# Kernel tuning notes

Measured on AMD Instinct MI355X. Metric: run time of the kernel, lower is better.

The kernel has to match this reference:

```python
import jax, jax.numpy as jnp
import numpy as np

DIM = 256
WS = 12          # window_size
NH = 8           # num_heads
HD = DIM // NH   # head_dim
NW = WS * WS     # tokens per window = 144


def _relative_position_index(ws: int) -> np.ndarray:
    coords = np.stack(np.meshgrid(np.arange(ws), np.arange(ws), indexing='ij'))  # [2, ws, ws]
    cf = coords.reshape(2, -1)                                  # [2, Nw]
    rel = cf[:, :, None] - cf[:, None, :]                       # [2, Nw, Nw]
    rel = rel.transpose(1, 2, 0).copy()                         # [Nw, Nw, 2]
    rel[:, :, 0] += ws - 1
    rel[:, :, 1] += ws - 1
    rel[:, :, 0] *= 2 * ws - 1
    return rel.sum(-1).astype(np.int32)                         # [Nw, Nw]


def setup_inputs() -> dict:
    key = jax.random.key(0)
    ks = jax.random.split(key, 6)
    BnW = 2048
    x = jax.random.normal(ks[0], (BnW, NW, DIM), dtype=jnp.float32)
    # weights stored as [in, out] (torch Linear applies x @ W.T + b)
    qkv_w = jax.random.normal(ks[1], (DIM, 3 * DIM), dtype=jnp.float32) * 0.02
    qkv_b = jnp.zeros((3 * DIM,), dtype=jnp.float32)
    proj_w = jax.random.normal(ks[2], (DIM, DIM), dtype=jnp.float32) * 0.02
    proj_b = jnp.zeros((DIM,), dtype=jnp.float32)
    rpb_table = jax.random.normal(ks[3], ((2 * WS - 1) ** 2, NH), dtype=jnp.float32) * 0.02
    rel_index = jnp.asarray(_relative_position_index(WS))       # [Nw, Nw] int32
    return {"x": x, "qkv_w": qkv_w, "qkv_b": qkv_b, "proj_w": proj_w,
            "proj_b": proj_b, "rpb_table": rpb_table, "rel_index": rel_index}


def reference(x, qkv_w, qkv_b, proj_w, proj_b, rpb_table, rel_index):
    BnW, Nw, C = x.shape
    scale = HD ** -0.5
    qkv = x @ qkv_w + qkv_b                                     # [BnW, Nw, 3C]
    qkv = qkv.reshape(BnW, Nw, 3, NH, HD)
    q, k, v = qkv[:, :, 0], qkv[:, :, 1], qkv[:, :, 2]          # [BnW, Nw, H, D]
    attn = jnp.einsum('bnhd,bmhd->bhnm', q * scale, k)          # [BnW, H, Nw, Nw]
    bias = rpb_table[rel_index]                                 # [Nw, Nw, H]
    attn = attn + jnp.transpose(bias, (2, 0, 1))[None]          # broadcast over BnW
    attn = jax.nn.softmax(attn, axis=-1)
    out = jnp.einsum('bhnm,bmhd->bnhd', attn, v).reshape(BnW, Nw, C)
    return out @ proj_w + proj_b
```

## Files before the change

kernel.cpp:

```cpp
#include <hip/hip_runtime.h>
#include <cstdint>
#include <cstddef>

#define NWIN 2048
#define NW   144
#define DIM  256
#define NHD  8
#define HD   32
#define MTOT (NWIN * NW)
#define SCALE 0.17677669529663687f

typedef __bf16 bf16x8 __attribute__((ext_vector_type(8)));
typedef float  f32x4  __attribute__((ext_vector_type(4)));
typedef unsigned short u16;
typedef unsigned short u16x4 __attribute__((ext_vector_type(4)));

__device__ __forceinline__ u16 f2bf(float f) {
  unsigned u = __float_as_uint(f);
  u += 0x7fffu + ((u >> 16) & 1u);
  return (u16)(u >> 16);
}

__device__ __forceinline__ bf16x8 pack8(f32x4 lo, f32x4 hi) {
  union { bf16x8 v; u16 u[8]; } o;
  o.u[0] = f2bf(lo.x); o.u[1] = f2bf(lo.y); o.u[2] = f2bf(lo.z); o.u[3] = f2bf(lo.w);
  o.u[4] = f2bf(hi.x); o.u[5] = f2bf(hi.y); o.u[6] = f2bf(hi.z); o.u[7] = f2bf(hi.w);
  return o.v;
}

__device__ __forceinline__ f32x4 mfma16(bf16x8 a, bf16x8 b, f32x4 c) {
  return __builtin_amdgcn_mfma_f32_16x16x32_bf16(a, b, c, 0, 0, 0);
}

__global__ void k_prep(const float* __restrict__ qkv_w, const float* __restrict__ proj_w,
                       const float* __restrict__ rpb, const int* __restrict__ rel,
                       u16* __restrict__ wqkvt, u16* __restrict__ wprojt,
                       float* __restrict__ biasar) {
  int tid = blockIdx.x * blockDim.x + threadIdx.x;
  int stride = gridDim.x * blockDim.x;
  for (int i = tid; i < 768 * 256; i += stride) {
    int n = i >> 8, k = i & 255;
    wqkvt[i] = f2bf(qkv_w[(size_t)k * 768 + n]);
  }
  for (int i = tid; i < 256 * 256; i += stride) {
    int n = i >> 8, k = i & 255;
    wprojt[i] = f2bf(proj_w[(size_t)k * 256 + n]);
  }
  for (int i = tid; i < NW * NW; i += stride) {
    int idv = rel[i];
#pragma unroll
    for (int hh = 0; hh < 8; ++hh) biasar[hh * (NW * NW) + i] = rpb[idv * 8 + hh];
  }
}

template <int NT, bool AF32, bool OUTF32>
__global__ __launch_bounds__(256) void k_gemm_bt(const void* __restrict__ Av,
                                                 const u16* __restrict__ Bt,
                                                 const float* __restrict__ bias,
                                                 void* __restrict__ outv) {
  constexpr int N = NT * 128;
  __shared__ __align__(16) u16 As[128 * 64];
  __shared__ __align__(16) u16 Bs[128 * 64];
  int tid = threadIdx.x;
  int wave = tid >> 6, lane = tid & 63;
  int ln = lane & 15, quad = lane >> 4;
  int wm = wave >> 1, wn = wave & 1;

  int bid = blockIdx.x;
  int xcd = bid & 7, slot = bid >> 3;
  int mt = xcd * 288 + slot / NT;
  int nt = slot % NT;
  int m0 = mt * 128, n0 = nt * 128;

  f32x4 zero4 = {0.f, 0.f, 0.f, 0.f};
  f32x4 acc[4][4];
#pragma unroll
  for (int i = 0; i < 4; ++i)
#pragma unroll
    for (int j = 0; j < 4; ++j) acc[i][j] = zero4;

  for (int kt = 0; kt < 4; ++kt) {
    int k0 = kt * 64;
    bf16x8 avs[4], bvs[4];
#pragma unroll
    for (int i = 0; i < 4; ++i) {
      int s = i * 256 + tid;
      int r = s >> 3, c = s & 7;
      if constexpr (AF32) {
        const float* Af = (const float*)Av;
        const float* p = &Af[(size_t)(m0 + r) * 256 + k0 + c * 8];
        f32x4 lo = *(const f32x4*)p;
        f32x4 hi = *(const f32x4*)(p + 4);
        avs[i] = pack8(lo, hi);
      } else {
        const u16* Ab = (const u16*)Av;
        avs[i] = *(const bf16x8*)&Ab[(size_t)(m0 + r) * 256 + k0 + c * 8];
      }
      bvs[i] = *(const bf16x8*)&Bt[(size_t)(n0 + r) * 256 + k0 + c * 8];
    }
    if (kt) __syncthreads();
#pragma unroll
    for (int i = 0; i < 4; ++i) {
      int s = i * 256 + tid;
      int r = s >> 3, c = s & 7;
      int dst = r * 64 + (((c ^ (r & 7))) << 3);
      *(bf16x8*)&As[dst] = avs[i];
      *(bf16x8*)&Bs[dst] = bvs[i];
    }
    __syncthreads();
#pragma unroll
    for (int ks = 0; ks < 2; ++ks) {
      bf16x8 af[4], bfr[4];
#pragma unroll
      for (int t = 0; t < 4; ++t) {
        int rowa = wm * 64 + t * 16 + ln;
        int rowb = wn * 64 + t * 16 + ln;
        int ca = ks * 4 + quad;
        af[t]  = *(const bf16x8*)&As[rowa * 64 + ((ca ^ (rowa & 7)) << 3)];
        bfr[t] = *(const bf16x8*)&Bs[rowb * 64 + ((ca ^ (rowb & 7)) << 3)];
      }
#pragma unroll
      for (int i = 0; i < 4; ++i)
#pragma unroll
        for (int j = 0; j < 4; ++j) acc[i][j] = mfma16(af[i], bfr[j], acc[i][j]);
    }
  }

#pragma unroll
  for (int j = 0; j < 4; ++j) {
    int col = n0 + wn * 64 + j * 16 + ln;
    float bv = bias[col];
#pragma unroll
    for (int i = 0; i < 4; ++i) {
      int rbase = m0 + wm * 64 + i * 16 + quad * 4;
      f32x4 a = acc[i][j];
      if constexpr (OUTF32) {
        float* out = (float*)outv;
#pragma unroll
        for (int r = 0; r < 4; ++r) out[(size_t)(rbase + r) * N + col] = a[r] + bv;
      } else {
        u16* out = (u16*)outv;
#pragma unroll
        for (int r = 0; r < 4; ++r) out[(size_t)(rbase + r) * N + col] = f2bf(a[r] + bv);
      }
    }
  }
}

__global__ __launch_bounds__(192, 3) void k_attn(const u16* __restrict__ qkv,
                                                 const float* __restrict__ bias_arr,
                                                 u16* __restrict__ attn_out) {
  __shared__ __align__(16) u16 SqSk[144 * 40 * 2];
  __shared__ __align__(16) u16 Sv[32 * 160];
  u16* Sq = SqSk;
  u16* Sk = SqSk + 144 * 40;
  u16* Sp = SqSk;

  int bid = blockIdx.x;
  int xcd = bid & 7, idx = bid >> 3;
  int w = xcd * 256 + (idx >> 3);
  int h = idx & 7;

  int tid = threadIdx.x;
  const u16* base = qkv + (size_t)w * (NW * 768);
  int qo = h * 32, ko = 256 + h * 32, vo = 512 + h * 32;

#pragma unroll
  for (int it = 0; it < 3; ++it) {
    int s = tid + it * 192;
    int r = s >> 2, c = (s & 3) << 3;
    *(bf16x8*)&Sq[r * 40 + c] = *(const bf16x8*)&base[(size_t)r * 768 + qo + c];
    *(bf16x8*)&Sk[r * 40 + c] = *(const bf16x8*)&base[(size_t)r * 768 + ko + c];
    bf16x8 vv = *(const bf16x8*)&base[(size_t)r * 768 + vo + c];
#pragma unroll
    for (int j = 0; j < 8; ++j) Sv[(c + j) * 160 + r] = ((u16*)&vv)[j];
  }
  for (int s = tid; s < 32 * 16; s += 192) {
    int d = s >> 4, m = 144 + (s & 15);
    Sv[d * 160 + m] = 0;
  }
  __syncthreads();

  int wv = tid >> 6;
  int lane = tid & 63, ln = lane & 15, quad = lane >> 4;

  f32x4 zero4 = {0.f, 0.f, 0.f, 0.f};
  f32x4 accs[3][9];
#pragma unroll
  for (int i = 0; i < 3; ++i)
#pragma unroll
    for (int j = 0; j < 9; ++j) accs[i][j] = zero4;

  bf16x8 aq[3];
#pragma unroll
  for (int mt = 0; mt < 3; ++mt) {
    int row = (wv * 3 + mt) * 16 + ln;
    aq[mt] = *(const bf16x8*)&Sq[row * 40 + quad * 8];
  }
#pragma unroll
  for (int j = 0; j < 9; ++j) {
    bf16x8 bk = *(const bf16x8*)&Sk[(j * 16 + ln) * 40 + quad * 8];
#pragma unroll
    for (int mt = 0; mt < 3; ++mt) accs[mt][j] = mfma16(aq[mt], bk, accs[mt][j]);
  }

  u16x4 pb[3][9];
  const float* bh = bias_arr + h * (NW * NW);
#pragma unroll
  for (int mt = 0; mt < 3; ++mt) {
#pragma unroll
    for (int r = 0; r < 4; ++r) {
      int n = (wv * 3 + mt) * 16 + quad * 4 + r;
      float sv[9];
      float mx = -3.0e38f;
#pragma unroll
      for (int j = 0; j < 9; ++j) {
        sv[j] = accs[mt][j][r] * SCALE + bh[n * 144 + j * 16 + ln];
        mx = fmaxf(mx, sv[j]);
      }
#pragma unroll
      for (int off = 1; off < 16; off <<= 1) mx = fmaxf(mx, __shfl_xor(mx, off));
      float sum = 0.f;
#pragma unroll
      for (int j = 0; j < 9; ++j) { sv[j] = __expf(sv[j] - mx); sum += sv[j]; }
#pragma unroll
      for (int off = 1; off < 16; off <<= 1) sum += __shfl_xor(sum, off);
      float inv = 1.f / sum;
#pragma unroll
      for (int j = 0; j < 9; ++j) pb[mt][j][r] = f2bf(sv[j] * inv);
    }
  }

  f32x4 acco[3][2];
#pragma unroll
  for (int i = 0; i < 3; ++i) { acco[i][0] = zero4; acco[i][1] = zero4; }

#pragma unroll
  for (int cc = 0; cc < 3; ++cc) {
    __syncthreads();
    int njj = (cc == 2) ? 2 : 4;
#pragma unroll
    for (int mt = 0; mt < 3; ++mt)
#pragma unroll
      for (int r = 0; r < 4; ++r) {
        int n = (wv * 3 + mt) * 16 + quad * 4 + r;
#pragma unroll
        for (int jj = 0; jj < 4; ++jj) {
          if (jj >= njj) break;
          int jg = cc * 4 + jj;
          u16 val;
          if (jg < 9) val = pb[mt][jg][r]; else val = (u16)0;
          Sp[n * 72 + jj * 16 + ln] = val;
        }
      }
    __syncthreads();
    int nks = (cc == 2) ? 1 : 2;
#pragma unroll
    for (int ks = 0; ks < 2; ++ks) {
      if (ks >= nks) break;
      int kg = cc * 64 + ks * 32;
      bf16x8 bv0 = *(const bf16x8*)&Sv[ln * 160 + kg + quad * 8];
      bf16x8 bv1 = *(const bf16x8*)&Sv[(16 + ln) * 160 + kg + quad * 8];
#pragma unroll
      for (int mt = 0; mt < 3; ++mt) {
        int row = (wv * 3 + mt) * 16 + ln;
        bf16x8 ap = *(const bf16x8*)&Sp[row * 72 + ks * 32 + quad * 8];
        acco[mt][0] = mfma16(ap, bv0, acco[mt][0]);
        acco[mt][1] = mfma16(ap, bv1, acco[mt][1]);
      }
    }
  }

  u16* op = attn_out + (size_t)w * (NW * 256) + h * 32;
#pragma unroll
  for (int mt = 0; mt < 3; ++mt)
#pragma unroll
    for (int d2 = 0; d2 < 2; ++d2) {
      f32x4 a = acco[mt][d2];
      int col = d2 * 16 + ln;
#pragma unroll
      for (int r = 0; r < 4; ++r) {
        int n = (wv * 3 + mt) * 16 + quad * 4 + r;
        op[(size_t)n * 256 + col] = f2bf(a[r]);
      }
    }
}

extern "C" void kernel_launch(void* const* d_in, const int* in_sizes, int n_in,
                              void* d_out, int out_size, void* d_ws, size_t ws_size,
                              hipStream_t stream) {
  const float* x      = (const float*)d_in[0];
  const float* qkv_w  = (const float*)d_in[1];
  const float* qkv_b  = (const float*)d_in[2];
  const float* proj_w = (const float*)d_in[3];
  const float* proj_b = (const float*)d_in[4];
  const float* rpb    = (const float*)d_in[5];
  const int*   rel    = (const int*)d_in[6];
  float* out = (float*)d_out;

  u16* qkv    = (u16*)d_ws;
  u16* attno  = qkv + (size_t)MTOT * 768;
  u16* wqkvt  = attno + (size_t)MTOT * 256;
  u16* wprojt = wqkvt + 768 * 256;
  float* biasar = (float*)(wprojt + 256 * 256);

  k_prep<<<256, 256, 0, stream>>>(qkv_w, proj_w, rpb, rel, wqkvt, wprojt, biasar);
  k_gemm_bt<6, true,  false><<<13824, 256, 0, stream>>>(x, wqkvt, qkv_b, (void*)qkv);
  k_attn<<<16384, 192, 0, stream>>>(qkv, biasar, attno);
  k_gemm_bt<2, false, true><<<4608, 256, 0, stream>>>(attno, wprojt, proj_b, (void*)out);
}
```

Baseline: 1.031 ms.

## Make both projection GEMMs persistent with register-resident weights and double-buffered A tiles

Replaces the per-tile GEMM kernel with a persistent 512-thread kernel. Each block handles nine consecutive 128-row tiles for a fixed 128-column slice. The weight fragments for the full K=256 are loaded once into registers, and the A tiles stream through a double-buffered 128 KB LDS buffer, with the global loads of the next tile overlapped with the current tile's MFMAs. The aim is to remove repeated B staging, per-tile launch overhead and load/compute serialization. In exchange it uses heavy LDS and register budgets, likely allowing only one block per CU and lowering occupancy.

```diff
diff --git a/kernel.cpp b/kernel.cpp
--- a/kernel.cpp
+++ b/kernel.cpp
@@ -54,13 +54,14 @@
 }
 
 template <int NT, bool AF32, bool OUTF32>
-__global__ __launch_bounds__(256) void k_gemm_bt(const void* __restrict__ Av,
-                                                 const u16* __restrict__ Bt,
-                                                 const float* __restrict__ bias,
-                                                 void* __restrict__ outv) {
+__global__ __launch_bounds__(512, 2) void k_gemm_persist(const void* __restrict__ Av,
+                                                         const u16* __restrict__ Bt,
+                                                         const float* __restrict__ bias,
+                                                         void* __restrict__ outv) {
   constexpr int N = NT * 128;
-  __shared__ __align__(16) u16 As[128 * 64];
-  __shared__ __align__(16) u16 Bs[128 * 64];
+  constexpr int TPB = 9;
+  __shared__ __align__(16) u16 As[2][128 * 256];
+
   int tid = threadIdx.x;
   int wave = tid >> 6, lane = tid & 63;
   int ln = lane & 15, quad = lane >> 4;
@@ -68,80 +69,142 @@
 
   int bid = blockIdx.x;
   int xcd = bid & 7, slot = bid >> 3;
-  int mt = xcd * 288 + slot / NT;
+  int g = xcd * 32 + slot / NT;
   int nt = slot % NT;
-  int m0 = mt * 128, n0 = nt * 128;
+  int n0 = nt * 128;
+  int m0base = g * (TPB * 128);
+
+  bf16x8 bfr[8][4];
+#pragma unroll
+  for (int ks = 0; ks < 8; ++ks)
+#pragma unroll
+    for (int j = 0; j < 4; ++j)
+      bfr[ks][j] = *(const bf16x8*)&Bt[(size_t)(n0 + wn * 64 + j * 16 + ln) * 256 + ks * 32 + quad * 8];
+
+#pragma unroll
+  for (int i = 0; i < 8; ++i) {
+    int p = i * 512 + tid;
+    int r = p >> 5, pc = p & 31;
+    bf16x8 v;
+    if constexpr (AF32) {
+      const float* ptr = &((const float*)Av)[(size_t)(m0base + r) * 256 + pc * 8];
+      v = pack8(*(const f32x4*)ptr, *(const f32x4*)(ptr + 4));
+    } else {
+      v = *(const bf16x8*)&((const u16*)Av)[(size_t)(m0base + r) * 256 + pc * 8];
+    }
+    *(bf16x8*)&As[0][r * 256 + ((pc ^ (r & 7)) << 3)] = v;
+  }
+  __syncthreads();
 
   f32x4 zero4 = {0.f, 0.f, 0.f, 0.f};
-  f32x4 acc[4][4];
-#pragma unroll
-  for (int i = 0; i < 4; ++i)
-#pragma unroll
-    for (int j = 0; j < 4; ++j) acc[i][j] = zero4;
-
-  for (int kt = 0; kt < 4; ++kt) {
-    int k0 = kt * 64;
-    bf16x8 avs[4], bvs[4];
-#pragma unroll
-    for (int i = 0; i < 4; ++i) {
-      int s = i * 256 + tid;
-      int r = s >> 3, c = s & 7;
-      if constexpr (AF32) {
-        const float* Af = (const float*)Av;
-        const float* p = &Af[(size_t)(m0 + r) * 256 + k0 + c * 8];
-        f32x4 lo = *(const f32x4*)p;
-        f32x4 hi = *(const f32x4*)(p + 4);
-        avs[i] = pack8(lo, hi);
-      } else {
-        const u16* Ab = (const u16*)Av;
-        avs[i] = *(const bf16x8*)&Ab[(size_t)(m0 + r) * 256 + k0 + c * 8];
-      }
-      bvs[i] = *(const bf16x8*)&Bt[(size_t)(n0 + r) * 256 + k0 + c * 8];
-    }
-    if (kt) __syncthreads();
-#pragma unroll
-    for (int i = 0; i < 4; ++i) {
-      int s = i * 256 + tid;
-      int r = s >> 3, c = s & 7;
-      int dst = r * 64 + (((c ^ (r & 7))) << 3);
-      *(bf16x8*)&As[dst] = avs[i];
-      *(bf16x8*)&Bs[dst] = bvs[i];
-    }
-    __syncthreads();
-#pragma unroll
-    for (int ks = 0; ks < 2; ++ks) {
-      bf16x8 af[4], bfr[4];
-#pragma unroll
-      for (int t = 0; t < 4; ++t) {
-        int rowa = wm * 64 + t * 16 + ln;
-        int rowb = wn * 64 + t * 16 + ln;
-        int ca = ks * 4 + quad;
-        af[t]  = *(const bf16x8*)&As[rowa * 64 + ((ca ^ (rowa & 7)) << 3)];
-        bfr[t] = *(const bf16x8*)&Bs[rowb * 64 + ((ca ^ (rowb & 7)) << 3)];
-      }
-#pragma unroll
-      for (int i = 0; i < 4; ++i)
-#pragma unroll
-        for (int j = 0; j < 4; ++j) acc[i][j] = mfma16(af[i], bfr[j], acc[i][j]);
-    }
-  }
-
-#pragma unroll
-  for (int j = 0; j < 4; ++j) {
-    int col = n0 + wn * 64 + j * 16 + ln;
-    float bv = bias[col];
-#pragma unroll
-    for (int i = 0; i < 4; ++i) {
-      int rbase = m0 + wm * 64 + i * 16 + quad * 4;
-      f32x4 a = acc[i][j];
-      if constexpr (OUTF32) {
-        float* out = (float*)outv;
-#pragma unroll
-        for (int r = 0; r < 4; ++r) out[(size_t)(rbase + r) * N + col] = a[r] + bv;
-      } else {
-        u16* out = (u16*)outv;
-#pragma unroll
-        for (int r = 0; r < 4; ++r) out[(size_t)(rbase + r) * N + col] = f2bf(a[r] + bv);
+
+  for (int t = 0; t < TPB; ++t) {
+    int cur = t & 1, nxt = cur ^ 1;
+    int m0 = m0base + t * 128;
+    bool hn = (t + 1 < TPB);
+    const u16* curs = &As[cur][0];
+    u16* nxts = &As[nxt][0];
+
+    f32x4 acc[2][4];
+#pragma unroll
+    for (int i = 0; i < 2; ++i)
+#pragma unroll
+      for (int j = 0; j < 4; ++j) acc[i][j] = zero4;
+
+    f32x4 lo[4], hi[4];
+    bf16x8 pv[4];
+
+    if (hn) {
+#pragma unroll
+      for (int i = 0; i < 4; ++i) {
+        int p = i * 512 + tid;
+        int r = p >> 5, pc = p & 31;
+        if constexpr (AF32) {
+          const float* ptr = &((const float*)Av)[(size_t)(m0 + 128 + r) * 256 + pc * 8];
+          lo[i] = *(const f32x4*)ptr; hi[i] = *(const f32x4*)(ptr + 4);
+        } else {
+          pv[i] = *(const bf16x8*)&((const u16*)Av)[(size_t)(m0 + 128 + r) * 256 + pc * 8];
+        }
+      }
+    }
+#pragma unroll
+    for (int ks = 0; ks < 4; ++ks) {
+      bf16x8 af[2];
+#pragma unroll
+      for (int i = 0; i < 2; ++i) {
+        int r = wm * 32 + i * 16 + ln;
+        af[i] = *(const bf16x8*)&curs[r * 256 + (((ks * 4 + quad) ^ (r & 7)) << 3)];
+      }
+#pragma unroll
+      for (int i = 0; i < 2; ++i)
+#pragma unroll
+        for (int j = 0; j < 4; ++j) acc[i][j] = mfma16(af[i], bfr[ks][j], acc[i][j]);
+    }
+    if (hn) {
+#pragma unroll
+      for (int i = 0; i < 4; ++i) {
+        int p = i * 512 + tid;
+        int r = p >> 5, pc = p & 31;
+        bf16x8 v;
+        if constexpr (AF32) v = pack8(lo[i], hi[i]); else v = pv[i];
+        *(bf16x8*)&nxts[r * 256 + ((pc ^ (r & 7)) << 3)] = v;
+      }
+    }
+    if (hn) {
+#pragma unroll
+      for (int i = 0; i < 4; ++i) {
+        int p = (4 + i) * 512 + tid;
+        int r = p >> 5, pc = p & 31;
+        if constexpr (AF32) {
+          const float* ptr = &((const float*)Av)[(size_t)(m0 + 128 + r) * 256 + pc * 8];
+          lo[i] = *(const f32x4*)ptr; hi[i] = *(const f32x4*)(ptr + 4);
+        } else {
+          pv[i] = *(const bf16x8*)&((const u16*)Av)[(size_t)(m0 + 128 + r) * 256 + pc * 8];
+        }
+      }
+    }
+#pragma unroll
+    for (int ks = 4; ks < 8; ++ks) {
+      bf16x8 af[2];
+#pragma unroll
+      for (int i = 0; i < 2; ++i) {
+        int r = wm * 32 + i * 16 + ln;
+        af[i] = *(const bf16x8*)&curs[r * 256 + (((ks * 4 + quad) ^ (r & 7)) << 3)];
+      }
+#pragma unroll
+      for (int i = 0; i < 2; ++i)
+#pragma unroll
+        for (int j = 0; j < 4; ++j) acc[i][j] = mfma16(af[i], bfr[ks][j], acc[i][j]);
+    }
+    if (hn) {
+#pragma unroll
+      for (int i = 0; i < 4; ++i) {
+        int p = (4 + i) * 512 + tid;
+        int r = p >> 5, pc = p & 31;
+        bf16x8 v;
+        if constexpr (AF32) v = pack8(lo[i], hi[i]); else v = pv[i];
+        *(bf16x8*)&nxts[r * 256 + ((pc ^ (r & 7)) << 3)] = v;
+      }
+    }
+    if (hn) __syncthreads();
+
+#pragma unroll
+    for (int j = 0; j < 4; ++j) {
+      int col = n0 + wn * 64 + j * 16 + ln;
+      float bv = bias[col];
+#pragma unroll
+      for (int i = 0; i < 2; ++i) {
+        int rbase = m0 + wm * 32 + i * 16 + quad * 4;
+        f32x4 a = acc[i][j];
+        if constexpr (OUTF32) {
+          float* out = (float*)outv;
+#pragma unroll
+          for (int r = 0; r < 4; ++r) out[(size_t)(rbase + r) * N + col] = a[r] + bv;
+        } else {
+          u16* out = (u16*)outv;
+#pragma unroll
+          for (int r = 0; r < 4; ++r) out[(size_t)(rbase + r) * N + col] = f2bf(a[r] + bv);
+        }
       }
     }
   }
@@ -305,7 +368,7 @@
   float* biasar = (float*)(wprojt + 256 * 256);
 
   k_prep<<<256, 256, 0, stream>>>(qkv_w, proj_w, rpb, rel, wqkvt, wprojt, biasar);
-  k_gemm_bt<6, true,  false><<<13824, 256, 0, stream>>>(x, wqkvt, qkv_b, (void*)qkv);
+  k_gemm_persist<6, true,  false><<<1536, 512, 0, stream>>>(x, wqkvt, qkv_b, (void*)qkv);
   k_attn<<<16384, 192, 0, stream>>>(qkv, biasar, attno);
-  k_gemm_bt<2, false, true><<<4608, 256, 0, stream>>>(attno, wprojt, proj_b, (void*)out);
-}
+  k_gemm_persist<2, false, true><<<512, 512, 0, stream>>>(attno, wprojt, proj_b, (void*)out);
+}
```

Result: no change. 1.028 ms (-0.3%).
